# Kernel optimization log

Hardware: AMD Instinct MI355X
Metric: run time of the kernel (lower is better)

## Reference

```python
import jax, jax.numpy as jnp
from jax import lax
import numpy as np

B, C, H, W = 32, 64, 80, 80


def setup_inputs() -> dict:
    key = jax.random.key(0)
    ks = jax.random.split(key, 9)
    x = jax.random.normal(ks[0], (B, C, H, W), dtype=jnp.float32)
    # gammas are zero-init Parameters in torch; use small random values so the
    # recurrence is non-trivial but numerically stable (spectral radius ~0.4).
    g = lambda k: jax.random.normal(k, (C, C), dtype=jnp.float32) * 0.05
    return {"x": x,
            "g1": g(ks[1]), "g2": g(ks[2]),
            "g4": g(ks[3]), "g5": g(ks[4]),
            "g7": g(ks[5]), "g8": g(ks[6]),
            "g10": g(ks[7]), "g11": g(ks[8])}


def _scan_dir(xh, gv, gh, apply_relu):
    """Row-major DAG recurrence over xh: [H, W, C, B].
    h[i,j] = act(x[i,j] + gv @ h[i-1,j] + gh @ h[i,j-1]).
    Zero carry at boundaries exactly reproduces the i>0 / j>0 guards
    (gamma @ 0 == 0)."""
    def row_step(prev_row, x_row):
        # prev_row: [W, C, B] -- vertical contribution for the whole row at once
        up = jnp.einsum('cd,wdb->wcb', gv, prev_row)
        def col_step(left, inp):
            xc, upc = inp                      # [C, B] each
            h = xc + upc + gh @ left
            if apply_relu:
                h = jax.nn.relu(h)
            return h, h
        _, row = lax.scan(col_step, jnp.zeros_like(x_row[0]), (x_row, up))
        return row, row
    _, out = lax.scan(row_step, jnp.zeros_like(xh[0]), xh)
    return out


def reference(x, g1, g2, g4, g5, g7, g8, g10, g11):
    # torch permutes to [C, B, H, W]; we use [H, W, C, B] so scans run over
    # leading axes and each cell is the same [C, B] matrix as hse[:, :, i, j].
    xh = jnp.transpose(x, (2, 3, 1, 0))  # [H, W, C, B]
    # SE: i forward, j forward, ReLU
    hse = _scan_dir(xh, g1, g2, True)
    # NE: i reversed, j forward, ReLU -> flip H
    hne = _scan_dir(xh[::-1], g4, g5, True)[::-1]
    # NW: i reversed, j reversed, ReLU -> flip H and W
    hnw = _scan_dir(xh[::-1, ::-1], g7, g8, True)[::-1, ::-1]
    # SW: i forward, j reversed, NO ReLU (omitted in the original code) -> flip W
    hsw = _scan_dir(xh[:, ::-1], g10, g11, False)[:, ::-1]
    out = hse + hne + hnw + hsw
    return jnp.transpose(out, (3, 2, 0, 1))  # back to [B, C, H, W]
```

## Files before the change

kernel.cpp:

```cpp
#include <hip/hip_runtime.h>
#include <stdint.h>

#define HH 80
#define WW 80
#define CC 64
#define BB 32
#define NDIAG (HH + WW - 1)
#define SLICE (HH * WW * CC)
#define NCW 5
#define NTHREADS (NCW * 64)

typedef _Float16 f16;
typedef _Float16 f16x8 __attribute__((ext_vector_type(8)));
typedef _Float16 f16x4 __attribute__((ext_vector_type(4)));
typedef float floatx4 __attribute__((ext_vector_type(4)));

struct GPtrs { const float* p[8]; };


__global__ __launch_bounds__(256) void xpose_kernel(const float* __restrict__ x,
                                                    f16* __restrict__ xT) {
  const int bi = blockIdx.x;
  const int b = bi / HH, i = bi - b * HH;
  __shared__ float tile[WW][CC + 1];
  const float* xp = x + ((size_t)(b * CC) * HH + i) * WW;
  for (int idx = threadIdx.x; idx < CC * WW; idx += 256) {
    const int c = idx / WW, j = idx - c * WW;
    tile[j][c] = xp[(size_t)c * (HH * WW) + j];
  }
  __syncthreads();
  f16* op = xT + (size_t)(b * HH + i) * WW * CC;
  for (int idx = threadIdx.x; idx < (WW * CC) / 4; idx += 256) {
    const int j = idx >> 4, m = idx & 15;
    const int cbase = 32 * ((m >> 1) & 1) + 8 * (m >> 2) + 4 * (m & 1);
    f16x4 v;
    v[0] = (f16)tile[j][cbase + 0];
    v[1] = (f16)tile[j][cbase + 1];
    v[2] = (f16)tile[j][cbase + 2];
    v[3] = (f16)tile[j][cbase + 3];
    *(f16x4*)(op + j * CC + m * 4) = v;
  }
}

__device__ inline f16x8 dpp_shr1(f16x8 v) {
  union { f16x8 h; int i[4]; } s, r;
  s.h = v;
#pragma unroll
  for (int k = 0; k < 4; ++k)
    r.i[k] = __builtin_amdgcn_update_dpp(0, s.i[k], 0x111, 0xF, 0xF, true);
  return r.h;
}

__global__ __launch_bounds__(NTHREADS, 1) void dag_kernel(const f16* __restrict__ xT,
                                                          GPtrs g,
                                                          f16* __restrict__ scratch) {
  const int blk = blockIdx.x;
  const int dir = blk >> 5;
  const int b   = blk & 31;
  const int tid = threadIdx.x;
  const int wv   = tid >> 6;
  const int lane = tid & 63;
  const int l15  = lane & 15;
  const int q    = lane >> 4;

  const bool fi      = (dir == 1) || (dir == 2);
  const bool fj      = (dir == 2) || (dir == 3);
  const bool do_relu = (dir != 3);
  const float* __restrict__ gv = g.p[2 * dir];
  const float* __restrict__ gh = g.p[2 * dir + 1];

  __align__(16) __shared__ f16 bnd[2][NCW][4][16];
  {
    f16x8 z = {};
    f16x8* bp = (f16x8*)&bnd[0][0][0][0];
    for (int idx = tid; idx < (2 * NCW * 4 * 16) / 8; idx += NTHREADS)
      bp[idx] = z;
  }

  const f16* const xTb = xT + (size_t)b * SLICE;
  f16* const sbase = scratch + (size_t)blk * SLICE;

  const int ip = wv * 16 + l15;
  const int io1 = fi ? (HH - 1 - ip) : ip;

  f16x8 Av[4][2], Ah[4][2];
#pragma unroll
  for (int cb = 0; cb < 4; ++cb) {
    const int row = 32 * (cb >> 1) + 8 * (l15 >> 2) + 4 * (cb & 1) + (l15 & 3);
    const float* pv = gv + row * CC;
    const float* ph = gh + row * CC;
#pragma unroll
    for (int jj = 0; jj < 8; ++jj) {
      Av[cb][0][jj] = (f16)pv[q * 8 + jj];
      Av[cb][1][jj] = (f16)pv[32 + q * 8 + jj];
      Ah[cb][0][jj] = (f16)ph[q * 8 + jj];
      Ah[cb][1][jj] = (f16)ph[32 + q * 8 + jj];
    }
  }

  f16x8 XA[2], XB[2];
  auto prefetch = [&](int dd, f16x8 (&X)[2]) {
    const int lo2 = max(0, dd - (WW - 1)), hi2 = min(dd, HH - 1);
    const int ipc = min(max(ip, lo2), hi2);
    const int jp2 = dd - ipc;
    const int io2 = fi ? (HH - 1 - ipc) : ipc;
    const int jo2 = fj ? (WW - 1 - jp2) : jp2;
    const f16* xp = xTb + (((size_t)(io2 * WW + jo2)) << 6) + q * 16;
    X[0] = *(const f16x8*)(xp);
    X[1] = *(const f16x8*)(xp + 8);
  };
  prefetch(0, XA);
  prefetch(1, XB);

  f16x8 P0 = {}, P1 = {};

  __syncthreads();

  auto step = [&](int d, f16x8 (&X)[2], int rdp, int wrp) {
    const int lo = max(0, d - (WW - 1));
    const int hi = min(d, HH - 1);
    const bool ok = (ip >= lo) && (ip <= hi);
    f16x8 BU0 = dpp_shr1(P0);
    f16x8 BU1 = dpp_shr1(P1);
    if (wv > 0) {
      const f16x8 b0 = *(const f16x8*)&bnd[rdp][wv - 1][q][0];
      const f16x8 b1 = *(const f16x8*)&bnd[rdp][wv - 1][q][8];
      if (l15 == 0) { BU0 = b0; BU1 = b1; }
    }
    floatx4 hs[4];
#pragma unroll
    for (int cb = 0; cb < 4; ++cb) {
      const f16x8 xs = (cb < 2) ? X[0] : X[1];
      const int eb = (cb & 1) * 4;
      floatx4 a1, a2;
      a1[0] = (float)xs[eb + 0]; a1[1] = (float)xs[eb + 1];
      a1[2] = (float)xs[eb + 2]; a1[3] = (float)xs[eb + 3];
      a2[0] = 0.f; a2[1] = 0.f; a2[2] = 0.f; a2[3] = 0.f;
      a1 = __builtin_amdgcn_mfma_f32_16x16x32_f16(Av[cb][0], BU0, a1, 0, 0, 0);
      a2 = __builtin_amdgcn_mfma_f32_16x16x32_f16(Ah[cb][0], P0,  a2, 0, 0, 0);
      a1 = __builtin_amdgcn_mfma_f32_16x16x32_f16(Av[cb][1], BU1, a1, 0, 0, 0);
      a2 = __builtin_amdgcn_mfma_f32_16x16x32_f16(Ah[cb][1], P1,  a2, 0, 0, 0);
      hs[cb][0] = a1[0] + a2[0]; hs[cb][1] = a1[1] + a2[1];
      hs[cb][2] = a1[2] + a2[2]; hs[cb][3] = a1[3] + a2[3];
    }
    if (do_relu) {
#pragma unroll
      for (int cb = 0; cb < 4; ++cb)
#pragma unroll
        for (int r = 0; r < 4; ++r) hs[cb][r] = fmaxf(hs[cb][r], 0.f);
    }
    f16x8 nP0, nP1;
#pragma unroll
    for (int r = 0; r < 4; ++r) {
      nP0[r]     = (f16)hs[0][r];
      nP0[4 + r] = (f16)hs[1][r];
      nP1[r]     = (f16)hs[2][r];
      nP1[4 + r] = (f16)hs[3][r];
    }
    const f16x8 z = {};
    P0 = ok ? nP0 : z;
    P1 = ok ? nP1 : z;
    if (l15 == 15) {
      *(f16x8*)&bnd[wrp][wv][q][0] = P0;
      *(f16x8*)&bnd[wrp][wv][q][8] = P1;
    }
    if (ok) {
      const int jp  = d - ip;
      const int jo1 = fj ? (WW - 1 - jp) : jp;
      f16* so = sbase + (((size_t)(io1 * WW + jo1)) << 6) + q * 16;
      *(f16x8*)(so)     = P0;
      *(f16x8*)(so + 8) = P1;
    }
    prefetch(min(d + 2, NDIAG - 1), X);
    __builtin_amdgcn_s_waitcnt(0xC07F);
    __builtin_amdgcn_s_barrier();
  };

  for (int d = 0; d < NDIAG - 1; d += 2) {
    step(d,     XA, 1, 0);
    step(d + 1, XB, 0, 1);
  }
  step(NDIAG - 1, XA, 1, 0);
}

__global__ __launch_bounds__(256) void reduce_kernel(const f16* __restrict__ s,
                                                     float* __restrict__ out) {
  const int bi = blockIdx.x;
  const int b = bi / HH, i = bi - b * HH;
  __shared__ float tile[WW][CC + 1];
  const size_t dstride = (size_t)BB * SLICE;
  const f16* p = s + (size_t)b * SLICE + (size_t)i * (WW * CC);
  for (int idx = threadIdx.x; idx < (WW * CC) / 8; idx += 256) {
    const int j = idx >> 3, k = idx & 7;
    const size_t off = (size_t)j * CC + k * 8;
    const f16x8 a0 = *(const f16x8*)(p + off);
    const f16x8 a1 = *(const f16x8*)(p + off + dstride);
    const f16x8 a2 = *(const f16x8*)(p + off + 2 * dstride);
    const f16x8 a3 = *(const f16x8*)(p + off + 3 * dstride);
    const int c0 = 32 * (k & 1) + 8 * (k >> 1);
#pragma unroll
    for (int t = 0; t < 8; ++t)
      tile[j][c0 + t] = (float)a0[t] + (float)a1[t] + (float)a2[t] + (float)a3[t];
  }
  __syncthreads();
  float* op = out + ((size_t)(b * CC) * HH + i) * WW;
  const int c  = threadIdx.x >> 2;
  const int jb = (threadIdx.x & 3) * 4;
#pragma unroll
  for (int k = 0; k < 5; ++k) {
    const int j0 = jb + k * 16;
    floatx4 v;
    v[0] = tile[j0 + 0][c];
    v[1] = tile[j0 + 1][c];
    v[2] = tile[j0 + 2][c];
    v[3] = tile[j0 + 3][c];
    *(floatx4*)(op + (size_t)c * (HH * WW) + j0) = v;
  }
}

extern "C" void kernel_launch(void* const* d_in, const int* in_sizes, int n_in,
                              void* d_out, int out_size, void* d_ws, size_t ws_size,
                              hipStream_t stream) {
  const float* x = (const float*)d_in[0];
  GPtrs g;
  for (int k = 0; k < 8; ++k) g.p[k] = (const float*)d_in[k + 1];
  f16* xT = (f16*)d_ws;
  f16* scratch = xT + (size_t)BB * SLICE;

  xpose_kernel<<<BB * HH, 256, 0, stream>>>(x, xT);
  dag_kernel<<<4 * BB, NTHREADS, 0, stream>>>((const f16*)xT, g, scratch);
  reduce_kernel<<<BB * HH, 256, 0, stream>>>((const f16*)scratch, (float*)d_out);
}
```

Baseline: 266.2 us.

## Replace per-diagonal workgroup barriers with LDS flag-based wavefront pipelining

Each wave now runs its own skewed range of 96 diagonals starting at wv*16, instead of all waves stepping through every diagonal together under a block barrier. Boundary rows pass between neighbouring waves through an 8-deep LDS ring, and per-wave progress flags are polled with atomic loads. The horizontal MFMA is issued before waiting on the upstream wave, so it can overlap the wait, and the prefetch depth grows from 2 to 4. This removes idle diagonal steps and barrier stalls, but relies on relaxed-ordering spin waits within the workgroup for correctness.

Measured after the change: 225.4 us. 15.3% less time.

```diff
diff --git a/kernel.cpp b/kernel.cpp
--- a/kernel.cpp
+++ b/kernel.cpp
@@ -9,6 +9,7 @@
 #define SLICE (HH * WW * CC)
 #define NCW 5
 #define NTHREADS (NCW * 64)
+#define RINGD 8
 
 typedef _Float16 f16;
 typedef _Float16 f16x8 __attribute__((ext_vector_type(8)));
@@ -69,19 +70,16 @@
   const float* __restrict__ gv = g.p[2 * dir];
   const float* __restrict__ gh = g.p[2 * dir + 1];
 
-  __align__(16) __shared__ f16 bnd[2][NCW][4][16];
-  {
-    f16x8 z = {};
-    f16x8* bp = (f16x8*)&bnd[0][0][0][0];
-    for (int idx = tid; idx < (2 * NCW * 4 * 16) / 8; idx += NTHREADS)
-      bp[idx] = z;
-  }
+  __align__(16) __shared__ f16 bnd[RINGD][NCW][4][16];
+  __shared__ int flags[NCW];
+  if (tid < NCW) flags[tid] = 16 * tid - 1;
 
   const f16* const xTb = xT + (size_t)b * SLICE;
   f16* const sbase = scratch + (size_t)blk * SLICE;
 
-  const int ip = wv * 16 + l15;
-  const int io1 = fi ? (HH - 1 - ip) : ip;
+  const int ip    = wv * 16 + l15;
+  const int io1   = fi ? (HH - 1 - ip) : ip;
+  const int dbase = wv * 16;
 
   f16x8 Av[4][2], Ah[4][2];
 #pragma unroll
@@ -98,7 +96,6 @@
     }
   }
 
-  f16x8 XA[2], XB[2];
   auto prefetch = [&](int dd, f16x8 (&X)[2]) {
     const int lo2 = max(0, dd - (WW - 1)), hi2 = min(dd, HH - 1);
     const int ipc = min(max(ip, lo2), hi2);
@@ -109,39 +106,62 @@
     X[0] = *(const f16x8*)(xp);
     X[1] = *(const f16x8*)(xp + 8);
   };
-  prefetch(0, XA);
-  prefetch(1, XB);
+
+  f16x8 X0[2], X1[2], X2[2], X3[2];
+  prefetch(dbase + 0, X0);
+  prefetch(dbase + 1, X1);
+  prefetch(dbase + 2, X2);
+  prefetch(dbase + 3, X3);
 
   f16x8 P0 = {}, P1 = {};
+  f16x8 SE0, SE1, SO0, SO1;
+  int fup = -0x40000000;
+  int fdn = -0x40000000;
 
   __syncthreads();
 
-  auto step = [&](int d, f16x8 (&X)[2], int rdp, int wrp) {
+  auto step = [&](int k, f16x8 (&X)[2], f16x8& S0, f16x8& S1) {
+    const int d  = dbase + k;
     const int lo = max(0, d - (WW - 1));
     const int hi = min(d, HH - 1);
     const bool ok = (ip >= lo) && (ip <= hi);
+
     f16x8 BU0 = dpp_shr1(P0);
     f16x8 BU1 = dpp_shr1(P1);
-    if (wv > 0) {
-      const f16x8 b0 = *(const f16x8*)&bnd[rdp][wv - 1][q][0];
-      const f16x8 b1 = *(const f16x8*)&bnd[rdp][wv - 1][q][8];
-      if (l15 == 0) { BU0 = b0; BU1 = b1; }
-    }
+
     floatx4 hs[4];
 #pragma unroll
     for (int cb = 0; cb < 4; ++cb) {
       const f16x8 xs = (cb < 2) ? X[0] : X[1];
       const int eb = (cb & 1) * 4;
-      floatx4 a1, a2;
-      a1[0] = (float)xs[eb + 0]; a1[1] = (float)xs[eb + 1];
-      a1[2] = (float)xs[eb + 2]; a1[3] = (float)xs[eb + 3];
-      a2[0] = 0.f; a2[1] = 0.f; a2[2] = 0.f; a2[3] = 0.f;
+      floatx4 a2;
+      a2[0] = (float)xs[eb + 0]; a2[1] = (float)xs[eb + 1];
+      a2[2] = (float)xs[eb + 2]; a2[3] = (float)xs[eb + 3];
+      a2 = __builtin_amdgcn_mfma_f32_16x16x32_f16(Ah[cb][0], P0, a2, 0, 0, 0);
+      a2 = __builtin_amdgcn_mfma_f32_16x16x32_f16(Ah[cb][1], P1, a2, 0, 0, 0);
+      hs[cb] = a2;
+    }
+
+    if (wv > 0 && k <= 79) {
+      if (fup < d - 1) {
+        do {
+          fup = __hip_atomic_load(&flags[wv - 1], __ATOMIC_RELAXED,
+                                  __HIP_MEMORY_SCOPE_WORKGROUP);
+        } while (fup < d - 1);
+      }
+      __builtin_amdgcn_sched_barrier(0);
+      const f16x8 b0 = *(const f16x8*)&bnd[(d - 1) & (RINGD - 1)][wv - 1][q][0];
+      const f16x8 b1 = *(const f16x8*)&bnd[(d - 1) & (RINGD - 1)][wv - 1][q][8];
+      if (l15 == 0) { BU0 = b0; BU1 = b1; }
+    }
+
+#pragma unroll
+    for (int cb = 0; cb < 4; ++cb) {
+      floatx4 a1 = {0.f, 0.f, 0.f, 0.f};
       a1 = __builtin_amdgcn_mfma_f32_16x16x32_f16(Av[cb][0], BU0, a1, 0, 0, 0);
-      a2 = __builtin_amdgcn_mfma_f32_16x16x32_f16(Ah[cb][0], P0,  a2, 0, 0, 0);
       a1 = __builtin_amdgcn_mfma_f32_16x16x32_f16(Av[cb][1], BU1, a1, 0, 0, 0);
-      a2 = __builtin_amdgcn_mfma_f32_16x16x32_f16(Ah[cb][1], P1,  a2, 0, 0, 0);
-      hs[cb][0] = a1[0] + a2[0]; hs[cb][1] = a1[1] + a2[1];
-      hs[cb][2] = a1[2] + a2[2]; hs[cb][3] = a1[3] + a2[3];
+      hs[cb][0] += a1[0]; hs[cb][1] += a1[1];
+      hs[cb][2] += a1[2]; hs[cb][3] += a1[3];
     }
     if (do_relu) {
 #pragma unroll
@@ -160,27 +180,43 @@
     const f16x8 z = {};
     P0 = ok ? nP0 : z;
     P1 = ok ? nP1 : z;
-    if (l15 == 15) {
-      *(f16x8*)&bnd[wrp][wv][q][0] = P0;
-      *(f16x8*)&bnd[wrp][wv][q][8] = P1;
-    }
+
+    if (wv < NCW - 1 && k >= 15 && k <= 94) {
+      if (fdn < d - (RINGD - 1)) {
+        do {
+          fdn = __hip_atomic_load(&flags[wv + 1], __ATOMIC_RELAXED,
+                                  __HIP_MEMORY_SCOPE_WORKGROUP);
+        } while (fdn < d - (RINGD - 1));
+      }
+      __builtin_amdgcn_sched_barrier(0);
+      if (l15 == 15) {
+        *(f16x8*)&bnd[d & (RINGD - 1)][wv][q][0] = P0;
+        *(f16x8*)&bnd[d & (RINGD - 1)][wv][q][8] = P1;
+      }
+    }
+    __builtin_amdgcn_s_waitcnt(0xC07F);
+    __builtin_amdgcn_sched_barrier(0);
+    if (lane == 0)
+      __hip_atomic_store(&flags[wv], d, __ATOMIC_RELAXED,
+                         __HIP_MEMORY_SCOPE_WORKGROUP);
+
     if (ok) {
+      S0 = P0; S1 = P1;
       const int jp  = d - ip;
       const int jo1 = fj ? (WW - 1 - jp) : jp;
       f16* so = sbase + (((size_t)(io1 * WW + jo1)) << 6) + q * 16;
-      *(f16x8*)(so)     = P0;
-      *(f16x8*)(so + 8) = P1;
-    }
-    prefetch(min(d + 2, NDIAG - 1), X);
-    __builtin_amdgcn_s_waitcnt(0xC07F);
-    __builtin_amdgcn_s_barrier();
+      *(f16x8*)(so)     = S0;
+      *(f16x8*)(so + 8) = S1;
+    }
+    prefetch(min(d + 4, NDIAG - 1), X);
   };
 
-  for (int d = 0; d < NDIAG - 1; d += 2) {
-    step(d,     XA, 1, 0);
-    step(d + 1, XB, 0, 1);
-  }
-  step(NDIAG - 1, XA, 1, 0);
+  for (int k = 0; k < 96; k += 4) {
+    step(k,     X0, SE0, SE1);
+    step(k + 1, X1, SO0, SO1);
+    step(k + 2, X2, SE0, SE1);
+    step(k + 3, X3, SO0, SO1);
+  }
 }
 
 __global__ __launch_bounds__(256) void reduce_kernel(const f16* __restrict__ s,
```

## Collapse DAG wavefront scan into single wave with register-resident row tiles

Applied to the files above, without the earlier changes.

The per-(direction,batch) block shrinks from five waves to one wave that holds all five 16-row tiles in registers. Cross-tile boundary values now move via DPP lane shifts instead of LDS writes and per-diagonal barriers, and the input x is added in fp16 after the MFMA instead of seeding the accumulator. This removes the barrier and LDS traffic on the critical path but serializes five tiles' MFMA chains into one wave, raises register pressure, and reduces precision slightly.

Measured after the change: 331.3 us. 24.5% more time.

```diff
diff --git a/kernel.cpp b/kernel.cpp
--- a/kernel.cpp
+++ b/kernel.cpp
@@ -7,8 +7,6 @@
 #define BB 32
 #define NDIAG (HH + WW - 1)
 #define SLICE (HH * WW * CC)
-#define NCW 5
-#define NTHREADS (NCW * 64)
 
 typedef _Float16 f16;
 typedef _Float16 f16x8 __attribute__((ext_vector_type(8)));
@@ -51,17 +49,29 @@
   return r.h;
 }
 
-__global__ __launch_bounds__(NTHREADS, 1) void dag_kernel(const f16* __restrict__ xT,
-                                                          GPtrs g,
-                                                          f16* __restrict__ scratch) {
+__device__ inline f16x8 dpp_shl15(f16x8 v) {
+  union { f16x8 h; int i[4]; } s, r;
+  s.h = v;
+#pragma unroll
+  for (int k = 0; k < 4; ++k)
+    r.i[k] = __builtin_amdgcn_update_dpp(0, s.i[k], 0x10F, 0xF, 0xF, true);
+  return r.h;
+}
+
+__device__ inline floatx4 MF(f16x8 a, f16x8 b, floatx4 c) {
+  return __builtin_amdgcn_mfma_f32_16x16x32_f16(a, b, c, 0, 0, 0);
+}
+
+__global__ __launch_bounds__(64, 1) void dag_kernel(const f16* __restrict__ xT,
+                                                    GPtrs g,
+                                                    f16* __restrict__ scratch) {
   const int blk = blockIdx.x;
   const int dir = blk >> 5;
   const int b   = blk & 31;
-  const int tid = threadIdx.x;
-  const int wv   = tid >> 6;
-  const int lane = tid & 63;
+  const int lane = threadIdx.x & 63;
   const int l15  = lane & 15;
   const int q    = lane >> 4;
+  const int q16  = q * 16;
 
   const bool fi      = (dir == 1) || (dir == 2);
   const bool fj      = (dir == 2) || (dir == 3);
@@ -69,19 +79,8 @@
   const float* __restrict__ gv = g.p[2 * dir];
   const float* __restrict__ gh = g.p[2 * dir + 1];
 
-  __align__(16) __shared__ f16 bnd[2][NCW][4][16];
-  {
-    f16x8 z = {};
-    f16x8* bp = (f16x8*)&bnd[0][0][0][0];
-    for (int idx = tid; idx < (2 * NCW * 4 * 16) / 8; idx += NTHREADS)
-      bp[idx] = z;
-  }
-
   const f16* const xTb = xT + (size_t)b * SLICE;
   f16* const sbase = scratch + (size_t)blk * SLICE;
-
-  const int ip = wv * 16 + l15;
-  const int io1 = fi ? (HH - 1 - ip) : ip;
 
   f16x8 Av[4][2], Ah[4][2];
 #pragma unroll
@@ -98,89 +97,105 @@
     }
   }
 
-  f16x8 XA[2], XB[2];
-  auto prefetch = [&](int dd, f16x8 (&X)[2]) {
-    const int lo2 = max(0, dd - (WW - 1)), hi2 = min(dd, HH - 1);
-    const int ipc = min(max(ip, lo2), hi2);
-    const int jp2 = dd - ipc;
-    const int io2 = fi ? (HH - 1 - ipc) : ipc;
-    const int jo2 = fj ? (WW - 1 - jp2) : jp2;
-    const f16* xp = xTb + (((size_t)(io2 * WW + jo2)) << 6) + q * 16;
-    X[0] = *(const f16x8*)(xp);
-    X[1] = *(const f16x8*)(xp + 8);
-  };
-  prefetch(0, XA);
-  prefetch(1, XB);
-
-  f16x8 P0 = {}, P1 = {};
-
-  __syncthreads();
-
-  auto step = [&](int d, f16x8 (&X)[2], int rdp, int wrp) {
+  int cbase[5];
+#pragma unroll
+  for (int t = 0; t < 5; ++t) {
+    const int ip = t * 16 + l15;
+    const int io = fi ? (HH - 1 - ip) : ip;
+    cbase[t] = io * WW + (fj ? (WW - 1 + ip) : -ip);
+  }
+
+  f16x8 P[5][2];
+  {
+    const f16x8 z = {};
+#pragma unroll
+    for (int t = 0; t < 5; ++t) { P[t][0] = z; P[t][1] = z; }
+  }
+
+  f16x8 XA[5][2], XB[5][2];
+  {
+    const int c0 = min(max(cbase[0], 0), HH * WW - 1);
+    const f16* xp0 = xTb + (((size_t)c0) << 6) + q16;
+    XA[0][0] = *(const f16x8*)xp0;  XA[0][1] = *(const f16x8*)(xp0 + 8);
+    const int c1 = min(max(cbase[0] + (fj ? -1 : 1), 0), HH * WW - 1);
+    const f16* xp1 = xTb + (((size_t)c1) << 6) + q16;
+    XB[0][0] = *(const f16x8*)xp1;  XB[0][1] = *(const f16x8*)(xp1 + 8);
+  }
+
+  auto step = [&](int d, f16x8 (&X)[5][2]) {
     const int lo = max(0, d - (WW - 1));
     const int hi = min(d, HH - 1);
-    const bool ok = (ip >= lo) && (ip <= hi);
-    f16x8 BU0 = dpp_shr1(P0);
-    f16x8 BU1 = dpp_shr1(P1);
-    if (wv > 0) {
-      const f16x8 b0 = *(const f16x8*)&bnd[rdp][wv - 1][q][0];
-      const f16x8 b1 = *(const f16x8*)&bnd[rdp][wv - 1][q][8];
-      if (l15 == 0) { BU0 = b0; BU1 = b1; }
+    const int tlo = lo >> 4, thi = hi >> 4;
+    const int sd = fj ? -d : d;
+    const int d2 = min(d + 2, NDIAG - 1);
+    const int lo2 = max(0, d2 - (WW - 1));
+    const int hi2 = min(d2, HH - 1);
+    const int tlo2 = lo2 >> 4, thi2 = hi2 >> 4;
+    const int sd2 = fj ? -d2 : d2;
+
+#define DO_TILE(T)                                                             \
+    if (tlo <= (T) && (T) <= thi) {                                            \
+      f16x8 BU0 = dpp_shr1(P[(T)][0]);                                         \
+      f16x8 BU1 = dpp_shr1(P[(T)][1]);                                         \
+      if ((T) > 0) {                                                           \
+        const f16x8 in0 = dpp_shl15(P[(T) > 0 ? (T) - 1 : 0][0]);              \
+        const f16x8 in1 = dpp_shl15(P[(T) > 0 ? (T) - 1 : 0][1]);              \
+        BU0 = (l15 == 0) ? in0 : BU0;                                          \
+        BU1 = (l15 == 0) ? in1 : BU1;                                          \
+      }                                                                        \
+      floatx4 a0 = {0.f, 0.f, 0.f, 0.f}, a1 = a0, a2 = a0, a3 = a0;            \
+      a0 = MF(Ah[0][0], P[(T)][0], a0); a1 = MF(Ah[1][0], P[(T)][0], a1);      \
+      a2 = MF(Ah[2][0], P[(T)][0], a2); a3 = MF(Ah[3][0], P[(T)][0], a3);      \
+      a0 = MF(Ah[0][1], P[(T)][1], a0); a1 = MF(Ah[1][1], P[(T)][1], a1);      \
+      a2 = MF(Ah[2][1], P[(T)][1], a2); a3 = MF(Ah[3][1], P[(T)][1], a3);      \
+      a0 = MF(Av[0][0], BU0, a0);       a1 = MF(Av[1][0], BU0, a1);            \
+      a2 = MF(Av[2][0], BU0, a2);       a3 = MF(Av[3][0], BU0, a3);            \
+      a0 = MF(Av[0][1], BU1, a0);       a1 = MF(Av[1][1], BU1, a1);            \
+      a2 = MF(Av[2][1], BU1, a2);       a3 = MF(Av[3][1], BU1, a3);            \
+      f16x8 r0, r1;                                                            \
+      _Pragma("unroll")                                                        \
+      for (int r = 0; r < 4; ++r) {                                            \
+        r0[r] = (f16)a0[r]; r0[4 + r] = (f16)a1[r];                            \
+        r1[r] = (f16)a2[r]; r1[4 + r] = (f16)a3[r];                            \
+      }                                                                        \
+      r0 = r0 + X[(T)][0];                \
+      r1 = r1 + X[(T)][1];                                                     \
+      if (do_relu) {                                                           \
+        _Pragma("unroll")                                                      \
+        for (int e = 0; e < 8; ++e) {                                          \
+          r0[e] = (r0[e] > (f16)0.f) ? r0[e] : (f16)0.f;                       \
+          r1[e] = (r1[e] > (f16)0.f) ? r1[e] : (f16)0.f;                       \
+        }                                                                      \
+      }                                                                        \
+      const bool ok = (l15 >= lo - (T) * 16) && (l15 <= hi - (T) * 16);        \
+      const f16x8 zz = {};                                                     \
+      P[(T)][0] = ok ? r0 : zz;                                                \
+      P[(T)][1] = ok ? r1 : zz;                                                \
+      if (ok) {                                                                \
+        f16* so = sbase + (((size_t)(cbase[(T)] + sd)) << 6) + q16;            \
+        *(f16x8*)so       = P[(T)][0];                                         \
+        *(f16x8*)(so + 8) = P[(T)][1];                                         \
+      }                                                                        \
     }
-    floatx4 hs[4];
-#pragma unroll
-    for (int cb = 0; cb < 4; ++cb) {
-      const f16x8 xs = (cb < 2) ? X[0] : X[1];
-      const int eb = (cb & 1) * 4;
-      floatx4 a1, a2;
-      a1[0] = (float)xs[eb + 0]; a1[1] = (float)xs[eb + 1];
-      a1[2] = (float)xs[eb + 2]; a1[3] = (float)xs[eb + 3];
-      a2[0] = 0.f; a2[1] = 0.f; a2[2] = 0.f; a2[3] = 0.f;
-      a1 = __builtin_amdgcn_mfma_f32_16x16x32_f16(Av[cb][0], BU0, a1, 0, 0, 0);
-      a2 = __builtin_amdgcn_mfma_f32_16x16x32_f16(Ah[cb][0], P0,  a2, 0, 0, 0);
-      a1 = __builtin_amdgcn_mfma_f32_16x16x32_f16(Av[cb][1], BU1, a1, 0, 0, 0);
-      a2 = __builtin_amdgcn_mfma_f32_16x16x32_f16(Ah[cb][1], P1,  a2, 0, 0, 0);
-      hs[cb][0] = a1[0] + a2[0]; hs[cb][1] = a1[1] + a2[1];
-      hs[cb][2] = a1[2] + a2[2]; hs[cb][3] = a1[3] + a2[3];
+    DO_TILE(4) DO_TILE(3) DO_TILE(2) DO_TILE(1) DO_TILE(0)
+#undef DO_TILE
+
+#define PF(T)                                                                  \
+    if (tlo2 <= (T) && (T) <= thi2) {                                          \
+      const int ci = min(max(cbase[(T)] + sd2, 0), HH * WW - 1);               \
+      const f16* xp = xTb + (((size_t)ci) << 6) + q16;                         \
+      X[(T)][0] = *(const f16x8*)xp;                                           \
+      X[(T)][1] = *(const f16x8*)(xp + 8);                                     \
     }
-    if (do_relu) {
-#pragma unroll
-      for (int cb = 0; cb < 4; ++cb)
-#pragma unroll
-        for (int r = 0; r < 4; ++r) hs[cb][r] = fmaxf(hs[cb][r], 0.f);
-    }
-    f16x8 nP0, nP1;
-#pragma unroll
-    for (int r = 0; r < 4; ++r) {
-      nP0[r]     = (f16)hs[0][r];
-      nP0[4 + r] = (f16)hs[1][r];
-      nP1[r]     = (f16)hs[2][r];
-      nP1[4 + r] = (f16)hs[3][r];
-    }
-    const f16x8 z = {};
-    P0 = ok ? nP0 : z;
-    P1 = ok ? nP1 : z;
-    if (l15 == 15) {
-      *(f16x8*)&bnd[wrp][wv][q][0] = P0;
-      *(f16x8*)&bnd[wrp][wv][q][8] = P1;
-    }
-    if (ok) {
-      const int jp  = d - ip;
-      const int jo1 = fj ? (WW - 1 - jp) : jp;
-      f16* so = sbase + (((size_t)(io1 * WW + jo1)) << 6) + q * 16;
-      *(f16x8*)(so)     = P0;
-      *(f16x8*)(so + 8) = P1;
-    }
-    prefetch(min(d + 2, NDIAG - 1), X);
-    __builtin_amdgcn_s_waitcnt(0xC07F);
-    __builtin_amdgcn_s_barrier();
+    PF(0) PF(1) PF(2) PF(3) PF(4)
+#undef PF
   };
 
   for (int d = 0; d < NDIAG - 1; d += 2) {
-    step(d,     XA, 1, 0);
-    step(d + 1, XB, 0, 1);
-  }
-  step(NDIAG - 1, XA, 1, 0);
+    step(d,     XA);
+    step(d + 1, XB);
+  }
+  step(NDIAG - 1, XA);
 }
 
 __global__ __launch_bounds__(256) void reduce_kernel(const f16* __restrict__ s,
@@ -228,6 +243,6 @@
   f16* scratch = xT + (size_t)BB * SLICE;
 
   xpose_kernel<<<BB * HH, 256, 0, stream>>>(x, xT);
-  dag_kernel<<<4 * BB, NTHREADS, 0, stream>>>((const f16*)xT, g, scratch);
+  dag_kernel<<<4 * BB, 64, 0, stream>>>((const f16*)xT, g, scratch);
   reduce_kernel<<<BB * HH, 256, 0, stream>>>((const f16*)scratch, (float*)d_out);
 }
```
